# Optimization experiments

Measured on AMD Instinct MI355X. Metric: run time of the kernel, lower is better.

The kernel has to match this reference:

```python
import jax, jax.numpy as jnp
import numpy as np

B, NPG, DEG = 512, 128, 16          # graphs, nodes/graph, out-degree
N = B * NPG                          # 65536 nodes
E = N * DEG                          # 1048576 edges
IN_DIM, HID, HEADS = 11, 32, 4
K1 = int(np.ceil(0.8 * NPG))         # 103 nodes/graph after pool1
K2 = int(np.ceil(0.8 * K1))          # 83 nodes/graph after pool2


def gat_conv(x, src, dst, mask, W, a_s, a_d, b, n_nodes):
    # PyG GATConv (concat=True, add_self_loops=True, eval mode -> no dropout)
    xp = (x @ W).reshape(n_nodes, HEADS, HID)            # [N,H,C]
    as_ = jnp.einsum('nhc,hc->nh', xp, a_s)
    ad_ = jnp.einsum('nhc,hc->nh', xp, a_d)
    loop = jnp.arange(n_nodes)
    s = jnp.concatenate([src, loop])
    d = jnp.concatenate([dst, loop])
    m = jnp.concatenate([mask, jnp.ones(n_nodes, bool)])
    logit = jax.nn.leaky_relu(as_[s] + ad_[d], 0.2)      # [E+N,H]
    logit = jnp.where(m[:, None], logit, -1e9)
    mx = jax.ops.segment_max(logit, d, num_segments=n_nodes)
    ex = jnp.exp(logit - mx[d]) * m[:, None]
    den = jax.ops.segment_sum(ex, d, num_segments=n_nodes)
    alpha = ex / (den[d] + 1e-16)                        # segment softmax over dst
    out = jax.ops.segment_sum(alpha[:, :, None] * xp[s], d, num_segments=n_nodes)
    return out.reshape(n_nodes, HEADS * HID) + b


def topk_pool(x, src, dst, mask, w, npg, k):
    # PyG TopKPooling: score = tanh((x*w).sum(-1)/||w||); keep top ceil(ratio*n) per graph
    nb = x.shape[0] // npg
    score = jnp.tanh((x @ w) / jnp.linalg.norm(w))
    vals, idx = jax.lax.top_k(score.reshape(nb, npg), k)  # [B,k]
    perm = (idx + (jnp.arange(nb) * npg)[:, None]).reshape(-1)
    x_new = x[perm] * vals.reshape(-1, 1)
    remap = jnp.full(nb * npg, -1).at[perm].set(jnp.arange(nb * k))
    ns, nd = remap[src], remap[dst]
    m = mask & (ns >= 0) & (nd >= 0)
    return x_new, jnp.where(m, ns, 0), jnp.where(m, nd, 0), m


def setup_inputs():
    key = jax.random.key(0)
    ks = jax.random.split(key, 24)
    s = 0.05
    x = jax.random.normal(ks[0], (N, IN_DIM), jnp.float32)
    src = jnp.repeat(jnp.arange(N), DEG)
    dst = (src // NPG) * NPG + jax.random.randint(ks[1], (E,), 0, NPG)
    edge_index = jnp.stack([src, dst])
    edge_attr = jax.random.normal(ks[2], (E, 4), jnp.float32)
    batch = jnp.repeat(jnp.arange(B), NPG)
    p = dict(
        W_g1=jax.random.normal(ks[3], (IN_DIM, HEADS * HID), jnp.float32) * s,
        att_src1=jax.random.normal(ks[4], (HEADS, HID), jnp.float32) * s,
        att_dst1=jax.random.normal(ks[5], (HEADS, HID), jnp.float32) * s,
        b_g1=jnp.zeros((HEADS * HID,), jnp.float32),
        W_t1=jax.random.normal(ks[6], (HEADS * HID, HID), jnp.float32) * s,
        b_t1=jnp.zeros((HID,), jnp.float32),
        pool_w1=jax.random.normal(ks[7], (HID,), jnp.float32) * s,
        W_g2=jax.random.normal(ks[8], (HID, HEADS * HID), jnp.float32) * s,
        att_src2=jax.random.normal(ks[9], (HEADS, HID), jnp.float32) * s,
        att_dst2=jax.random.normal(ks[10], (HEADS, HID), jnp.float32) * s,
        b_g2=jnp.zeros((HEADS * HID,), jnp.float32),
        W_t2=jax.random.normal(ks[11], (HEADS * HID, HID), jnp.float32) * s,
        b_t2=jnp.zeros((HID,), jnp.float32),
        pool_w2=jax.random.normal(ks[12], (HID,), jnp.float32) * s,
        W_l1=jax.random.normal(ks[13], (2 * HID, 256), jnp.float32) * s,
        b_l1=jnp.zeros((256,), jnp.float32),
        W_l2=jax.random.normal(ks[14], (256, 1024), jnp.float32) * s,
        b_l2=jnp.zeros((1024,), jnp.float32),
        W_l3=jax.random.normal(ks[15], (1024, 1), jnp.float32) * s,
        b_l3=jnp.zeros((1,), jnp.float32),
    )
    return dict(x=x, edge_index=edge_index, edge_attr=edge_attr, batch=batch, **p)


def reference(x, edge_index, edge_attr, batch,
              W_g1, att_src1, att_dst1, b_g1, W_t1, b_t1, pool_w1,
              W_g2, att_src2, att_dst2, b_g2, W_t2, b_t2, pool_w2,
              W_l1, b_l1, W_l2, b_l2, W_l3, b_l3):
    # edge_attr is ignored (GATConv built without edge_dim); batch is implicit
    # in the fixed equal-size graph layout.  Eval mode -> dropout disabled.
    src, dst = edge_index[0], edge_index[1]
    mask = jnp.ones(E, bool)
    h = jax.nn.relu(gat_conv(x, src, dst, mask, W_g1, att_src1, att_dst1, b_g1, N))
    h = h @ W_t1 + b_t1
    h, src, dst, mask = topk_pool(h, src, dst, mask, pool_w1, NPG, K1)
    h1 = h.reshape(B, K1, HID)
    g1 = jnp.concatenate([h1.max(1), h1.mean(1)], axis=1)   # [B, 2*HID]
    h = jax.nn.relu(gat_conv(h, src, dst, mask, W_g2, att_src2, att_dst2, b_g2, B * K1))
    h = h @ W_t2 + b_t2
    h, src, dst, mask = topk_pool(h, src, dst, mask, pool_w2, K1, K2)
    h2 = h.reshape(B, K2, HID)
    g2 = jnp.concatenate([h2.max(1), h2.mean(1)], axis=1)
    g = g1 + g2
    g = jax.nn.relu(g @ W_l1 + b_l1)
    g = jax.nn.relu(g @ W_l2 + b_l2)
    return g @ W_l3 + b_l3                                   # [B,1]
```

## Files before the change

### kernel.cpp

```cpp
#include <hip/hip_runtime.h>
#include <math.h>

constexpr int NPGc  = 128;
constexpr int NG    = 512;
constexpr int EPGc  = 2048;
constexpr int ETOT  = 1048576;
constexpr int IND   = 11;
constexpr int HIDc  = 32;
constexpr int FD    = 128;
constexpr int K1c   = 103;
constexpr int K2c   = 83;
constexpr int NN    = NG * NPGc;
constexpr int N2c   = NG * K1c;

__device__ __forceinline__ float lrelu(float x){ return fmaxf(x, 0.2f*x); }

__device__ __forceinline__ unsigned flipF(float f){
    unsigned u = __float_as_uint(f);
    return u ^ (unsigned)(((int)u >> 31) | 0x80000000);
}
__device__ __forceinline__ float unflipF(unsigned u){
    unsigned m = ((u >> 31) - 1u) | 0x80000000u;
    return __uint_as_float(u ^ m);
}

template<int KIN>
__device__ void foldDev(const float* __restrict__ Wg, const float* __restrict__ avs,
                        const float* __restrict__ avd, float* __restrict__ S, float* __restrict__ D, int t)
{
    if (t < KIN * 4) {
        int k = t >> 2, h = t & 3;
        float s = 0.f, d = 0.f;
        for (int j = 0; j < HIDc; j++) {
            float w = Wg[k*FD + h*HIDc + j];
            s = fmaf(w, avs[h*HIDc + j], s);
            d = fmaf(w, avd[h*HIDc + j], d);
        }
        S[t] = s; D[t] = d;
    }
}
__global__ void k_fold2(const float* W1, const float* s1, const float* d1, float* S1, float* D1,
                        const float* W2, const float* s2, const float* d2, float* S2, float* D2)
{
    if (blockIdx.x == 0) foldDev<IND>(W1, s1, d1, S1, D1, threadIdx.x);
    else                 foldDev<HIDc>(W2, s2, d2, S2, D2, threadIdx.x);
}

template<bool REMAP>
__global__ __launch_bounds__(256) void k_csr(const int* __restrict__ ei, const int* __restrict__ rankv,
                                             int* __restrict__ csrOff, unsigned char* __restrict__ csrSB,
                                             unsigned char* __restrict__ csrDB, int nnode)
{
    int g = blockIdx.x, t = threadIdx.x;
    __shared__ int cnt[128], cur[128], offL[129];
    __shared__ unsigned char sbL[EPGc], dbL[EPGc];
    __shared__ signed char rmap[NPGc];
    if (t < 128) cnt[t] = 0;
    if constexpr (REMAP) { if (t < NPGc) rmap[t] = (signed char)rankv[g*NPGc + t]; }
    __syncthreads();
    const int* dstG = ei + ETOT + g * EPGc;
    int sn[8], dn[8];
    #pragma unroll
    for (int q = 0; q < 8; q++) {
        int e = t + 256*q;
        int dO = dstG[e] - g * NPGc, s0 = e >> 4;
        if constexpr (REMAP) {
            int s = rmap[s0], d = rmap[dO];
            bool ok = (s >= 0 && d >= 0);
            sn[q] = s; dn[q] = ok ? d : -1;
        } else { sn[q] = s0; dn[q] = dO; }
        if (dn[q] >= 0) atomicAdd(&cnt[dn[q]], 1);
    }
    __syncthreads();
    if (t < 64) {
        int c0 = cnt[2*t], c1 = cnt[2*t + 1], ps = c0 + c1, P = ps;
        #pragma unroll
        for (int dlt = 1; dlt < 64; dlt <<= 1) { int v = __shfl_up(P, dlt); if (t >= dlt) P += v; }
        int E0 = P - ps;
        offL[2*t] = E0; offL[2*t + 1] = E0 + c0;
        cur[2*t] = E0; cur[2*t + 1] = E0 + c0;
        if (t == 63) offL[128] = P;
    }
    __syncthreads();
    #pragma unroll
    for (int q = 0; q < 8; q++) {
        if (dn[q] >= 0) {
            int pos = atomicAdd(&cur[dn[q]], 1);
            sbL[pos] = (unsigned char)sn[q];
            dbL[pos] = (unsigned char)dn[q];
        }
    }
    __syncthreads();
    if (t < 128) {
        ((int4*)(csrSB + (size_t)g * EPGc))[t] = ((const int4*)sbL)[t];
        ((int4*)(csrDB + (size_t)g * EPGc))[t] = ((const int4*)dbL)[t];
    }
    if (t <= nnode) csrOff[g*132 + t] = offL[t];
}

template<int NNODE, int KIN, int KEEP, bool FIRST>
__global__ __launch_bounds__(256, 4) void k_layer(
    const float* __restrict__ xin, const float* __restrict__ Wg,
    const float* __restrict__ WsS, const float* __restrict__ WsD,
    const float* __restrict__ bg,
    const float* __restrict__ Wt, const float* __restrict__ bt,
    const float* __restrict__ pw,
    const int* __restrict__ csrOff, const unsigned char* __restrict__ csrSB,
    const unsigned char* __restrict__ csrDB,
    float* __restrict__ xnew, int* __restrict__ rankv,
    float* __restrict__ gfeat, const float* __restrict__ gprev)
{
    constexpr int NP   = (NNODE + 3) & ~3;
    constexpr int NGRP = NP / 4;
    int g = blockIdx.x, t = threadIdx.x;

    __shared__ __align__(16) float xFT[KIN * NP];
    __shared__ __align__(16) float WfL[KIN * FD];
    __shared__ __align__(16) float WtL[FD * HIDc];
    __shared__ __align__(16) float xpL[NP * 36];
    __shared__ float wEu[EPGc];
    __shared__ unsigned char sbL[EPGc], dbL[EPGc];
    __shared__ int offL[NNODE + 1];
    __shared__ float asL[NNODE], adL[NNODE], sfW[NNODE], sDi[NNODE];
    __shared__ unsigned maxU[NNODE];
    __shared__ __align__(8) float admL[NNODE * 2];
    __shared__ float WsSL[KIN * 4], WsDL[KIN * 4], bgL[FD], btL[HIDc];

    {
        const float* xg = xin + (size_t)g * NNODE * KIN;
        for (int i = t; i < NNODE * KIN; i += 256) {
            int n = i / KIN, k = i - n * KIN;
            xFT[k * NP + n] = xg[i];
        }
        if constexpr (NP > NNODE) {
            for (int i = t; i < KIN * (NP - NNODE); i += 256) {
                int k = i / (NP - NNODE), n = NNODE + (i % (NP - NNODE));
                xFT[k * NP + n] = 0.f;
            }
        }
    }
    for (int i = t; i < KIN * FD / 4; i += 256) ((float4*)WfL)[i] = ((const float4*)Wg)[i];
    for (int i = t; i < FD * HIDc / 4; i += 256) ((float4*)WtL)[i] = ((const float4*)Wt)[i];
    for (int i = t; i < KIN * 4; i += 256) { WsSL[i] = WsS[i]; WsDL[i] = WsD[i]; }
    if (t < FD) bgL[t] = bg[t];
    if (t < HIDc) btL[t] = bt[t];
    if (t <= NNODE) offL[t] = csrOff[g*132 + t];
    for (int i = t; i < EPGc / 16; i += 256) {
        ((int4*)sbL)[i] = ((const int4*)(csrSB + (size_t)g * EPGc))[i];
        ((int4*)dbL)[i] = ((const int4*)(csrDB + (size_t)g * EPGc))[i];
    }
    __syncthreads();
    const int EC = offL[NNODE];

    const int n4 = t >> 3, j4 = t & 7;
    float4 acc0, acc1, acc2, acc3;
    { float4 bi = make_float4(btL[j4*4], btL[j4*4+1], btL[j4*4+2], btL[j4*4+3]);
      acc0 = bi; acc1 = bi; acc2 = bi; acc3 = bi; }

    for (int h = 0; h < 4; h++) {
        __syncthreads();

        for (int id = t; id < NGRP * 32; id += 256) {
            int grp = id >> 5, c = id & 31;
            float4 a = make_float4(0.f, 0.f, 0.f, 0.f);
            #pragma unroll
            for (int k = 0; k < KIN; k++) {
                float4 xv = *(const float4*)&xFT[k * NP + grp * 4];
                float w = WfL[k * FD + h * 32 + c];
                a.x = fmaf(xv.x, w, a.x); a.y = fmaf(xv.y, w, a.y);
                a.z = fmaf(xv.z, w, a.z); a.w = fmaf(xv.w, w, a.w);
            }
            int nb = grp * 4;
            xpL[(nb+0)*36 + c] = a.x; xpL[(nb+1)*36 + c] = a.y;
            xpL[(nb+2)*36 + c] = a.z; xpL[(nb+3)*36 + c] = a.w;
        }
        if (t < NNODE) {
            float s = 0.f, d = 0.f;
            #pragma unroll
            for (int k = 0; k < KIN; k++) {
                float v = xFT[k * NP + t];
                s = fmaf(v, WsSL[k*4 + h], s);
                d = fmaf(v, WsDL[k*4 + h], d);
            }
            asL[t] = s; adL[t] = d; maxU[t] = flipF(s);
        }
        __syncthreads();

        for (int s = t; s < EC; s += 256)
            atomicMax(&maxU[dbL[s]], flipF(asL[sbL[s]]));
        __syncthreads();

        if (t < NNODE) {
            float ad = adL[t];
            float m = lrelu(unflipF(maxU[t]) + ad);
            admL[2*t] = ad; admL[2*t + 1] = m;
            sfW[t] = expf(lrelu(asL[t] + ad) - m);
        }
        __syncthreads();

        for (int s = t; s < EC; s += 256) {
            int sb = sbL[s], db = dbL[s];
            float2 am = *(const float2*)&admL[2*db];
            wEu[s] = expf(lrelu(asL[sb] + am.x) - am.y);
        }
        __syncthreads();

        if (t < NNODE) {
            float den = sfW[t];
            int lo = offL[t], hi = offL[t + 1];
            for (int s = lo; s < hi; s++) den += wEu[s];
            sDi[t] = 1.f / (den + 1e-16f);
        }
        __syncthreads();

        const float4* X4 = (const float4*)xpL;
        auto aggOne = [&](int p) -> float4 {
            int n = p >> 3, c4 = p & 7;
            float w0 = sfW[n];
            float4 v = X4[n*9 + c4];
            float4 a; a.x = w0*v.x; a.y = w0*v.y; a.z = w0*v.z; a.w = w0*v.w;
            int lo = offL[n], hi = offL[n + 1];
            for (int s = lo; s < hi; s++) {
                int sc = sbL[s]; float w = wEu[s];
                float4 u = X4[sc*9 + c4];
                a.x = fmaf(w, u.x, a.x); a.y = fmaf(w, u.y, a.y);
                a.z = fmaf(w, u.z, a.z); a.w = fmaf(w, u.w, a.w);
            }
            float inv = sDi[n];
            float4 r;
            r.x = fmaxf(fmaf(a.x, inv, bgL[h*32 + c4*4 + 0]), 0.f);
            r.y = fmaxf(fmaf(a.y, inv, bgL[h*32 + c4*4 + 1]), 0.f);
            r.z = fmaxf(fmaf(a.z, inv, bgL[h*32 + c4*4 + 2]), 0.f);
            r.w = fmaxf(fmaf(a.w, inv, bgL[h*32 + c4*4 + 3]), 0.f);
            return r;
        };
        float4 rv0 = aggOne(t);
        float4 rv1 = aggOne(t + 256);
        float4 rv2 = aggOne(t + 512);
        float4 rv3;
        if (t + 768 < NNODE * 8) rv3 = aggOne(t + 768);
        __syncthreads();

        float4* X4w = (float4*)xpL;
        X4w[(t>>3)*9 + (t&7)] = rv0;
        { int p = t + 256; X4w[(p>>3)*9 + (p&7)] = rv1; }
        { int p = t + 512; X4w[(p>>3)*9 + (p&7)] = rv2; }
        if (t + 768 < NNODE * 8) { int p = t + 768; X4w[(p>>3)*9 + (p&7)] = rv3; }
        __syncthreads();

        if (n4 < NGRP) {
            int nb = n4 * 4;
            #pragma unroll 8
            for (int c = 0; c < 32; c++) {
                float4 w4 = *(const float4*)&WtL[(h*32 + c)*HIDc + j4*4];
                float r0 = xpL[(nb+0)*36 + c], r1 = xpL[(nb+1)*36 + c];
                float r2 = xpL[(nb+2)*36 + c], r3 = xpL[(nb+3)*36 + c];
                acc0.x = fmaf(r0, w4.x, acc0.x); acc0.y = fmaf(r0, w4.y, acc0.y);
                acc0.z = fmaf(r0, w4.z, acc0.z); acc0.w = fmaf(r0, w4.w, acc0.w);
                acc1.x = fmaf(r1, w4.x, acc1.x); acc1.y = fmaf(r1, w4.y, acc1.y);
                acc1.z = fmaf(r1, w4.z, acc1.z); acc1.w = fmaf(r1, w4.w, acc1.w);
                acc2.x = fmaf(r2, w4.x, acc2.x); acc2.y = fmaf(r2, w4.y, acc2.y);
                acc2.z = fmaf(r2, w4.z, acc2.z); acc2.w = fmaf(r2, w4.w, acc2.w);
                acc3.x = fmaf(r3, w4.x, acc3.x); acc3.y = fmaf(r3, w4.y, acc3.y);
                acc3.z = fmaf(r3, w4.z, acc3.z); acc3.w = fmaf(r3, w4.w, acc3.w);
            }
        }
    }
    __syncthreads();

    float* htL = xpL;
    if (n4 < NGRP) {
        int nb = n4 * 4, jb = j4 * 4;
        float4 av[4] = {acc0, acc1, acc2, acc3};
        #pragma unroll
        for (int i = 0; i < 4; i++) {
            int n = nb + i;
            if (n < NNODE) {
                htL[n*33 + jb + 0] = av[i].x; htL[n*33 + jb + 1] = av[i].y;
                htL[n*33 + jb + 2] = av[i].z; htL[n*33 + jb + 3] = av[i].w;
            }
        }
    }
    __syncthreads();

    float* scoreL = wEu;
    int*   rnkL   = (int*)(wEu + 128);
    float nrm; { float ss = 0.f; for (int k = 0; k < HIDc; k++) { float w = pw[k]; ss = fmaf(w, w, ss); } nrm = sqrtf(ss); }
    if (t < NNODE) {
        float dot = 0.f;
        for (int k = 0; k < HIDc; k++) dot = fmaf(htL[t*33 + k], pw[k], dot);
        scoreL[t] = tanhf(dot / nrm);
    }
    __syncthreads();
    if (t < NNODE) {
        float si = scoreL[t]; int rank = 0;
        for (int q = 0; q < NNODE; q++) {
            float sj = scoreL[q];
            rank += (sj > si || (sj == si && q < t)) ? 1 : 0;
        }
        rnkL[t] = (rank < KEEP) ? rank : -1;
        if (FIRST) rankv[g*NPGc + t] = rnkL[t];
    }
    __syncthreads();
    if (FIRST) {
        for (int p = t; p < NNODE * 32; p += 256) {
            int n = p >> 5, jj = p & 31;
            int rk = rnkL[n];
            if (rk >= 0) xnew[((size_t)g*KEEP + rk)*HIDc + jj] = htL[n*33 + jj] * scoreL[n];
        }
    }
    if (t < HIDc) {
        float mx = -INFINITY, sm = 0.f;
        for (int n = 0; n < NNODE; n++) {
            if (rnkL[n] >= 0) { float v = htL[n*33 + t] * scoreL[n]; mx = fmaxf(mx, v); sm += v; }
        }
        float mean = sm / (float)KEEP;
        if (FIRST) {
            gfeat[(size_t)g*64 + t]      = mx;
            gfeat[(size_t)g*64 + 32 + t] = mean;
        } else {
            gfeat[(size_t)g*64 + t]      = gprev[(size_t)g*64 + t] + mx;
            gfeat[(size_t)g*64 + 32 + t] = gprev[(size_t)g*64 + 32 + t] + mean;
        }
    }
}

__global__ __launch_bounds__(256) void k_mlpA(const float* __restrict__ gsum,
    const float* __restrict__ W1, const float* __restrict__ b1,
    const float* __restrict__ W2, const float* __restrict__ b2,
    const float* __restrict__ W3, float* __restrict__ part)
{
    int gb = blockIdx.x, q = blockIdx.y, t = threadIdx.x;
    int g0 = gb * 4;
    __shared__ float gL[256];
    __shared__ float h1L[1024];
    __shared__ float4 red[256];
    gL[t] = gsum[(size_t)g0*64 + t];
    __syncthreads();
    float bv = b1[t];
    float a0 = bv, a1 = bv, a2 = bv, a3 = bv;
    #pragma unroll 4
    for (int k = 0; k < 64; k++) {
        float w = W1[k*256 + t];
        a0 = fmaf(gL[k], w, a0); a1 = fmaf(gL[64 + k], w, a1);
        a2 = fmaf(gL[128 + k], w, a2); a3 = fmaf(gL[192 + k], w, a3);
    }
    h1L[t] = fmaxf(a0, 0.f); h1L[256 + t] = fmaxf(a1, 0.f);
    h1L[512 + t] = fmaxf(a2, 0.f); h1L[768 + t] = fmaxf(a3, 0.f);
    __syncthreads();
    int o = q * 256 + t;
    float b2v = b2[o], w3 = W3[o];
    float c0 = b2v, c1 = b2v, c2 = b2v, c3 = b2v;
    const float* w2c = W2 + o;
    #pragma unroll 8
    for (int i = 0; i < 256; i++) {
        float w = w2c[(size_t)i * 1024];
        c0 = fmaf(h1L[i], w, c0); c1 = fmaf(h1L[256 + i], w, c1);
        c2 = fmaf(h1L[512 + i], w, c2); c3 = fmaf(h1L[768 + i], w, c3);
    }
    red[t] = make_float4(fmaxf(c0, 0.f)*w3, fmaxf(c1, 0.f)*w3, fmaxf(c2, 0.f)*w3, fmaxf(c3, 0.f)*w3);
    __syncthreads();
    for (int s = 128; s > 0; s >>= 1) {
        if (t < s) { float4 a = red[t], b = red[t + s]; a.x += b.x; a.y += b.y; a.z += b.z; a.w += b.w; red[t] = a; }
        __syncthreads();
    }
    if (t == 0) {
        float4 r = red[0];
        part[(size_t)(g0 + 0)*4 + q] = r.x;
        part[(size_t)(g0 + 1)*4 + q] = r.y;
        part[(size_t)(g0 + 2)*4 + q] = r.z;
        part[(size_t)(g0 + 3)*4 + q] = r.w;
    }
}

__global__ void k_mlpB(const float* __restrict__ part, const float* __restrict__ b3,
                       float* __restrict__ outp)
{
    int g = blockIdx.x * 256 + threadIdx.x;
    if (g < NG) {
        float4 p = ((const float4*)part)[g];
        outp[g] = ((p.x + p.y) + (p.z + p.w)) + b3[0];
    }
}

extern "C" void kernel_launch(void* const* d_in, const int* in_sizes, int n_in,
                              void* d_out, int out_size, void* d_ws, size_t ws_size,
                              hipStream_t stream)
{
    const float* x    = (const float*)d_in[0];
    const int*   ei   = (const int*)  d_in[1];
    const float* W_g1 = (const float*)d_in[4];
    const float* as1w = (const float*)d_in[5];
    const float* ad1w = (const float*)d_in[6];
    const float* b_g1 = (const float*)d_in[7];
    const float* W_t1 = (const float*)d_in[8];
    const float* b_t1 = (const float*)d_in[9];
    const float* pw1  = (const float*)d_in[10];
    const float* W_g2 = (const float*)d_in[11];
    const float* as2w = (const float*)d_in[12];
    const float* ad2w = (const float*)d_in[13];
    const float* b_g2 = (const float*)d_in[14];
    const float* W_t2 = (const float*)d_in[15];
    const float* b_t2 = (const float*)d_in[16];
    const float* pw2  = (const float*)d_in[17];
    const float* W_l1 = (const float*)d_in[18];
    const float* b_l1 = (const float*)d_in[19];
    const float* W_l2 = (const float*)d_in[20];
    const float* b_l2 = (const float*)d_in[21];
    const float* W_l3 = (const float*)d_in[22];
    const float* b_l3 = (const float*)d_in[23];
    float* out = (float*)d_out;

    char* ws = (char*)d_ws;
    size_t off = 0;
    auto alloc = [&](size_t bytes) -> void* {
        void* p = (void*)(ws + off);
        off += ((bytes + 255) / 256) * 256;
        return p;
    };
    float* x2    = (float*)alloc((size_t)N2c * HIDc * 4);
    int*   rank1 = (int*)  alloc((size_t)NN * 4);
    float* g1    = (float*)alloc((size_t)NG * 64 * 4);
    float* gsum  = (float*)alloc((size_t)NG * 64 * 4);
    float* part  = (float*)alloc((size_t)NG * 4 * 4);
    float* wsS1  = (float*)alloc(64 * 4);
    float* wsD1  = (float*)alloc(64 * 4);
    float* wsS2  = (float*)alloc(128 * 4);
    float* wsD2  = (float*)alloc(128 * 4);
    int*   off1  = (int*)  alloc((size_t)NG * 132 * 4);
    unsigned char* sb1 = (unsigned char*)alloc((size_t)NG * EPGc);
    unsigned char* db1 = (unsigned char*)alloc((size_t)NG * EPGc);
    int*   off2  = (int*)  alloc((size_t)NG * 132 * 4);
    unsigned char* sb2 = (unsigned char*)alloc((size_t)NG * EPGc);
    unsigned char* db2 = (unsigned char*)alloc((size_t)NG * EPGc);

    k_fold2<<<2, 128, 0, stream>>>(W_g1, as1w, ad1w, wsS1, wsD1,
                                   W_g2, as2w, ad2w, wsS2, wsD2);
    k_csr<false><<<NG, 256, 0, stream>>>(ei, nullptr, off1, sb1, db1, NPGc);

    k_layer<NPGc, IND, K1c, true><<<NG, 256, 0, stream>>>(
        x, W_g1, wsS1, wsD1, b_g1, W_t1, b_t1, pw1,
        off1, sb1, db1, x2, rank1, g1, nullptr);

    k_csr<true><<<NG, 256, 0, stream>>>(ei, rank1, off2, sb2, db2, K1c);

    k_layer<K1c, HIDc, K2c, false><<<NG, 256, 0, stream>>>(
        x2, W_g2, wsS2, wsD2, b_g2, W_t2, b_t2, pw2,
        off2, sb2, db2, nullptr, nullptr, gsum, g1);

    k_mlpA<<<dim3(NG/4, 4), 256, 0, stream>>>(gsum, W_l1, b_l1, W_l2, b_l2, W_l3, part);
    k_mlpB<<<2, 256, 0, stream>>>(part, b_l3, out);
}
```

Baseline: 315.2 us.

## Fuse CSR build, pooled CSR remap, and MLP head into layer kernels

Merges the weight-fold and first CSR build into one launch, moves the second (remapped) CSR build into the first layer kernel's tail using the in-shared-memory ranks, and folds the MLP head into the second layer kernel per graph. This removes four kernel launches and the global round-trips for rank and gsum/part buffers. In exchange, the MLP now runs one graph per block, so each block rereads the whole 256x1024 W2 matrix (from cache) with less reuse than the previous 4-graph batching. It also adds shared-memory pressure and a longer tail to the layer kernels.

New measurement: 305.8 us. -3.0%, faster.

```diff
diff --git a/kernel.cpp b/kernel.cpp
--- a/kernel.cpp
+++ b/kernel.cpp
@@ -39,63 +39,56 @@
         S[t] = s; D[t] = d;
     }
 }
-__global__ void k_fold2(const float* W1, const float* s1, const float* d1, float* S1, float* D1,
-                        const float* W2, const float* s2, const float* d2, float* S2, float* D2)
+
+__global__ __launch_bounds__(256) void k_prep(const int* __restrict__ ei,
+    const float* __restrict__ W1g, const float* __restrict__ s1, const float* __restrict__ d1,
+    const float* __restrict__ W2g, const float* __restrict__ s2, const float* __restrict__ d2,
+    int* __restrict__ csrOff, unsigned char* __restrict__ csrSB, unsigned char* __restrict__ csrDB,
+    float* __restrict__ S1, float* __restrict__ D1, float* __restrict__ S2, float* __restrict__ D2)
 {
-    if (blockIdx.x == 0) foldDev<IND>(W1, s1, d1, S1, D1, threadIdx.x);
-    else                 foldDev<HIDc>(W2, s2, d2, S2, D2, threadIdx.x);
-}
-
-template<bool REMAP>
-__global__ __launch_bounds__(256) void k_csr(const int* __restrict__ ei, const int* __restrict__ rankv,
-                                             int* __restrict__ csrOff, unsigned char* __restrict__ csrSB,
-                                             unsigned char* __restrict__ csrDB, int nnode)
-{
-    int g = blockIdx.x, t = threadIdx.x;
+    int b = blockIdx.x, t = threadIdx.x;
+    if (b >= NG) {
+        if (b == NG)     foldDev<IND>(W1g, s1, d1, S1, D1, t);
+        else             foldDev<HIDc>(W2g, s2, d2, S2, D2, t);
+        return;
+    }
+    int g = b;
     __shared__ int cnt[128], cur[128], offL[129];
     __shared__ unsigned char sbL[EPGc], dbL[EPGc];
-    __shared__ signed char rmap[NPGc];
     if (t < 128) cnt[t] = 0;
-    if constexpr (REMAP) { if (t < NPGc) rmap[t] = (signed char)rankv[g*NPGc + t]; }
     __syncthreads();
     const int* dstG = ei + ETOT + g * EPGc;
-    int sn[8], dn[8];
+    int dnv[8];
     #pragma unroll
     for (int q = 0; q < 8; q++) {
         int e = t + 256*q;
-        int dO = dstG[e] - g * NPGc, s0 = e >> 4;
-        if constexpr (REMAP) {
-            int s = rmap[s0], d = rmap[dO];
-            bool ok = (s >= 0 && d >= 0);
-            sn[q] = s; dn[q] = ok ? d : -1;
-        } else { sn[q] = s0; dn[q] = dO; }
-        if (dn[q] >= 0) atomicAdd(&cnt[dn[q]], 1);
+        dnv[q] = dstG[e] - g * NPGc;
+        atomicAdd(&cnt[dnv[q]], 1);
     }
     __syncthreads();
     if (t < 64) {
         int c0 = cnt[2*t], c1 = cnt[2*t + 1], ps = c0 + c1, P = ps;
         #pragma unroll
-        for (int dlt = 1; dlt < 64; dlt <<= 1) { int v = __shfl_up(P, dlt); if (t >= dlt) P += v; }
+        for (int dl = 1; dl < 64; dl <<= 1) { int v = __shfl_up(P, dl); if (t >= dl) P += v; }
         int E0 = P - ps;
         offL[2*t] = E0; offL[2*t + 1] = E0 + c0;
-        cur[2*t] = E0; cur[2*t + 1] = E0 + c0;
+        cur[2*t]  = E0; cur[2*t + 1]  = E0 + c0;
         if (t == 63) offL[128] = P;
     }
     __syncthreads();
     #pragma unroll
     for (int q = 0; q < 8; q++) {
-        if (dn[q] >= 0) {
-            int pos = atomicAdd(&cur[dn[q]], 1);
-            sbL[pos] = (unsigned char)sn[q];
-            dbL[pos] = (unsigned char)dn[q];
-        }
+        int e = t + 256*q;
+        int pos = atomicAdd(&cur[dnv[q]], 1);
+        sbL[pos] = (unsigned char)(e >> 4);
+        dbL[pos] = (unsigned char)dnv[q];
     }
     __syncthreads();
     if (t < 128) {
         ((int4*)(csrSB + (size_t)g * EPGc))[t] = ((const int4*)sbL)[t];
         ((int4*)(csrDB + (size_t)g * EPGc))[t] = ((const int4*)dbL)[t];
     }
-    if (t <= nnode) csrOff[g*132 + t] = offL[t];
+    if (t <= NPGc) csrOff[g*132 + t] = offL[t];
 }
 
 template<int NNODE, int KIN, int KEEP, bool FIRST>
@@ -107,8 +100,15 @@
     const float* __restrict__ pw,
     const int* __restrict__ csrOff, const unsigned char* __restrict__ csrSB,
     const unsigned char* __restrict__ csrDB,
-    float* __restrict__ xnew, int* __restrict__ rankv,
-    float* __restrict__ gfeat, const float* __restrict__ gprev)
+    const int* __restrict__ ei,
+    int* __restrict__ csrOffW, unsigned char* __restrict__ sbW,
+    unsigned char* __restrict__ dbW,
+    float* __restrict__ xnew,
+    float* __restrict__ gfeat, const float* __restrict__ gprev,
+    const float* __restrict__ W1, const float* __restrict__ b1,
+    const float* __restrict__ W2, const float* __restrict__ b2,
+    const float* __restrict__ W3, const float* __restrict__ b3,
+    float* __restrict__ outp)
 {
     constexpr int NP   = (NNODE + 3) & ~3;
     constexpr int NGRP = NP / 4;
@@ -120,11 +120,12 @@
     __shared__ __align__(16) float xpL[NP * 36];
     __shared__ float wEu[EPGc];
     __shared__ unsigned char sbL[EPGc], dbL[EPGc];
-    __shared__ int offL[NNODE + 1];
+    __shared__ int offL[NNODE + 1 > 129 ? NNODE + 1 : 129];
     __shared__ float asL[NNODE], adL[NNODE], sfW[NNODE], sDi[NNODE];
     __shared__ unsigned maxU[NNODE];
     __shared__ __align__(8) float admL[NNODE * 2];
     __shared__ float WsSL[KIN * 4], WsDL[KIN * 4], bgL[FD], btL[HIDc];
+    __shared__ float gvec[64];
 
     {
         const float* xg = xin + (size_t)g * NNODE * KIN;
@@ -299,10 +300,9 @@
             rank += (sj > si || (sj == si && q < t)) ? 1 : 0;
         }
         rnkL[t] = (rank < KEEP) ? rank : -1;
-        if (FIRST) rankv[g*NPGc + t] = rnkL[t];
-    }
-    __syncthreads();
-    if (FIRST) {
+    }
+    __syncthreads();
+    if constexpr (FIRST) {
         for (int p = t; p < NNODE * 32; p += 256) {
             int n = p >> 5, jj = p & 31;
             int rk = rnkL[n];
@@ -315,71 +315,84 @@
             if (rnkL[n] >= 0) { float v = htL[n*33 + t] * scoreL[n]; mx = fmaxf(mx, v); sm += v; }
         }
         float mean = sm / (float)KEEP;
-        if (FIRST) {
+        if constexpr (FIRST) {
             gfeat[(size_t)g*64 + t]      = mx;
             gfeat[(size_t)g*64 + 32 + t] = mean;
         } else {
-            gfeat[(size_t)g*64 + t]      = gprev[(size_t)g*64 + t] + mx;
-            gfeat[(size_t)g*64 + 32 + t] = gprev[(size_t)g*64 + 32 + t] + mean;
-        }
-    }
-}
-
-__global__ __launch_bounds__(256) void k_mlpA(const float* __restrict__ gsum,
-    const float* __restrict__ W1, const float* __restrict__ b1,
-    const float* __restrict__ W2, const float* __restrict__ b2,
-    const float* __restrict__ W3, float* __restrict__ part)
-{
-    int gb = blockIdx.x, q = blockIdx.y, t = threadIdx.x;
-    int g0 = gb * 4;
-    __shared__ float gL[256];
-    __shared__ float h1L[1024];
-    __shared__ float4 red[256];
-    gL[t] = gsum[(size_t)g0*64 + t];
-    __syncthreads();
-    float bv = b1[t];
-    float a0 = bv, a1 = bv, a2 = bv, a3 = bv;
-    #pragma unroll 4
-    for (int k = 0; k < 64; k++) {
-        float w = W1[k*256 + t];
-        a0 = fmaf(gL[k], w, a0); a1 = fmaf(gL[64 + k], w, a1);
-        a2 = fmaf(gL[128 + k], w, a2); a3 = fmaf(gL[192 + k], w, a3);
-    }
-    h1L[t] = fmaxf(a0, 0.f); h1L[256 + t] = fmaxf(a1, 0.f);
-    h1L[512 + t] = fmaxf(a2, 0.f); h1L[768 + t] = fmaxf(a3, 0.f);
-    __syncthreads();
-    int o = q * 256 + t;
-    float b2v = b2[o], w3 = W3[o];
-    float c0 = b2v, c1 = b2v, c2 = b2v, c3 = b2v;
-    const float* w2c = W2 + o;
-    #pragma unroll 8
-    for (int i = 0; i < 256; i++) {
-        float w = w2c[(size_t)i * 1024];
-        c0 = fmaf(h1L[i], w, c0); c1 = fmaf(h1L[256 + i], w, c1);
-        c2 = fmaf(h1L[512 + i], w, c2); c3 = fmaf(h1L[768 + i], w, c3);
-    }
-    red[t] = make_float4(fmaxf(c0, 0.f)*w3, fmaxf(c1, 0.f)*w3, fmaxf(c2, 0.f)*w3, fmaxf(c3, 0.f)*w3);
-    __syncthreads();
-    for (int s = 128; s > 0; s >>= 1) {
-        if (t < s) { float4 a = red[t], b = red[t + s]; a.x += b.x; a.y += b.y; a.z += b.z; a.w += b.w; red[t] = a; }
-        __syncthreads();
-    }
-    if (t == 0) {
-        float4 r = red[0];
-        part[(size_t)(g0 + 0)*4 + q] = r.x;
-        part[(size_t)(g0 + 1)*4 + q] = r.y;
-        part[(size_t)(g0 + 2)*4 + q] = r.z;
-        part[(size_t)(g0 + 3)*4 + q] = r.w;
-    }
-}
-
-__global__ void k_mlpB(const float* __restrict__ part, const float* __restrict__ b3,
-                       float* __restrict__ outp)
-{
-    int g = blockIdx.x * 256 + threadIdx.x;
-    if (g < NG) {
-        float4 p = ((const float4*)part)[g];
-        outp[g] = ((p.x + p.y) + (p.z + p.w)) + b3[0];
+            gvec[t]      = gprev[(size_t)g*64 + t] + mx;
+            gvec[32 + t] = gprev[(size_t)g*64 + 32 + t] + mean;
+        }
+    }
+
+    if constexpr (FIRST) {
+        __syncthreads();
+        int* cnt = (int*)maxU;
+        int* cur = (int*)sfW;
+        if (t < 128) cnt[t] = 0;
+        __syncthreads();
+        const int* dstG = ei + ETOT + g * EPGc;
+        int snv[8], dnv[8];
+        #pragma unroll
+        for (int q = 0; q < 8; q++) {
+            int e = t + 256*q;
+            int s = rnkL[e >> 4], d = rnkL[dstG[e] - g * NPGc];
+            bool ok = (s >= 0 && d >= 0);
+            snv[q] = s; dnv[q] = ok ? d : -1;
+            if (ok) atomicAdd(&cnt[d], 1);
+        }
+        __syncthreads();
+        if (t < 64) {
+            int c0 = cnt[2*t], c1 = cnt[2*t + 1], ps = c0 + c1, P = ps;
+            #pragma unroll
+            for (int dl = 1; dl < 64; dl <<= 1) { int v = __shfl_up(P, dl); if (t >= dl) P += v; }
+            int E0 = P - ps;
+            offL[2*t] = E0; offL[2*t + 1] = E0 + c0;
+            cur[2*t]  = E0; cur[2*t + 1]  = E0 + c0;
+            if (t == 63) offL[128] = P;
+        }
+        __syncthreads();
+        #pragma unroll
+        for (int q = 0; q < 8; q++) {
+            if (dnv[q] >= 0) {
+                int pos = atomicAdd(&cur[dnv[q]], 1);
+                sbL[pos] = (unsigned char)snv[q];
+                dbL[pos] = (unsigned char)dnv[q];
+            }
+        }
+        __syncthreads();
+        if (t < 128) {
+            ((int4*)(sbW + (size_t)g * EPGc))[t] = ((const int4*)sbL)[t];
+            ((int4*)(dbW + (size_t)g * EPGc))[t] = ((const int4*)dbL)[t];
+        }
+        if (t <= K1c) csrOffW[g*132 + t] = offL[t];
+    } else {
+        __syncthreads();
+        float* h1L = wEu;
+        float* red = wEu + 256;
+        float a = b1[t];
+        #pragma unroll 4
+        for (int k = 0; k < 64; k++) a = fmaf(gvec[k], W1[k*256 + t], a);
+        h1L[t] = fmaxf(a, 0.f);
+        __syncthreads();
+        float c0 = b2[t], c1 = b2[t + 256], c2 = b2[t + 512], c3 = b2[t + 768];
+        const float* w2c = W2 + t;
+        #pragma unroll 4
+        for (int i = 0; i < 256; i++) {
+            float hv = h1L[i];
+            const float* wr = w2c + (size_t)i * 1024;
+            c0 = fmaf(hv, wr[0],   c0);
+            c1 = fmaf(hv, wr[256], c1);
+            c2 = fmaf(hv, wr[512], c2);
+            c3 = fmaf(hv, wr[768], c3);
+        }
+        float p = fmaf(fmaxf(c0, 0.f), W3[t],
+                  fmaf(fmaxf(c1, 0.f), W3[t + 256],
+                  fmaf(fmaxf(c2, 0.f), W3[t + 512],
+                       fmaxf(c3, 0.f) * W3[t + 768])));
+        red[t] = p;
+        __syncthreads();
+        for (int s = 128; s > 0; s >>= 1) { if (t < s) red[t] += red[t + s]; __syncthreads(); }
+        if (t == 0) outp[g] = red[0] + b3[0];
     }
 }
 
@@ -419,10 +432,7 @@
         return p;
     };
     float* x2    = (float*)alloc((size_t)N2c * HIDc * 4);
-    int*   rank1 = (int*)  alloc((size_t)NN * 4);
     float* g1    = (float*)alloc((size_t)NG * 64 * 4);
-    float* gsum  = (float*)alloc((size_t)NG * 64 * 4);
-    float* part  = (float*)alloc((size_t)NG * 4 * 4);
     float* wsS1  = (float*)alloc(64 * 4);
     float* wsD1  = (float*)alloc(64 * 4);
     float* wsS2  = (float*)alloc(128 * 4);
@@ -434,20 +444,20 @@
     unsigned char* sb2 = (unsigned char*)alloc((size_t)NG * EPGc);
     unsigned char* db2 = (unsigned char*)alloc((size_t)NG * EPGc);
 
-    k_fold2<<<2, 128, 0, stream>>>(W_g1, as1w, ad1w, wsS1, wsD1,
-                                   W_g2, as2w, ad2w, wsS2, wsD2);
-    k_csr<false><<<NG, 256, 0, stream>>>(ei, nullptr, off1, sb1, db1, NPGc);
+    k_prep<<<NG + 2, 256, 0, stream>>>(ei, W_g1, as1w, ad1w, W_g2, as2w, ad2w,
+                                       off1, sb1, db1, wsS1, wsD1, wsS2, wsD2);
 
     k_layer<NPGc, IND, K1c, true><<<NG, 256, 0, stream>>>(
         x, W_g1, wsS1, wsD1, b_g1, W_t1, b_t1, pw1,
-        off1, sb1, db1, x2, rank1, g1, nullptr);
-
-    k_csr<true><<<NG, 256, 0, stream>>>(ei, rank1, off2, sb2, db2, K1c);
+        off1, sb1, db1,
+        ei, off2, sb2, db2,
+        x2, g1, nullptr,
+        nullptr, nullptr, nullptr, nullptr, nullptr, nullptr, nullptr);
 
     k_layer<K1c, HIDc, K2c, false><<<NG, 256, 0, stream>>>(
         x2, W_g2, wsS2, wsD2, b_g2, W_t2, b_t2, pw2,
-        off2, sb2, db2, nullptr, nullptr, gsum, g1);
-
-    k_mlpA<<<dim3(NG/4, 4), 256, 0, stream>>>(gsum, W_l1, b_l1, W_l2, b_l2, W_l3, part);
-    k_mlpB<<<2, 256, 0, stream>>>(part, b_l3, out);
-}
+        off2, sb2, db2,
+        nullptr, nullptr, nullptr, nullptr,
+        nullptr, nullptr, g1,
+        W_l1, b_l1, W_l2, b_l2, W_l3, b_l3, out);
+}
```
